# Kernel optimization log

Hardware: AMD Instinct MI355X
Metric: run time of the kernel (lower is better)

Reference implementation:

```python
import jax, jax.numpy as jnp
import numpy as np

N_EMBD = 1024  # C in forward; scale uses C**-0.5

def setup_inputs() -> dict:
    key = jax.random.key(0)
    k1, k2, k3, k4 = jax.random.split(key, 4)
    B, T, C, H = 4, 4096, N_EMBD, 64
    x = jax.random.normal(k1, (B, T, C), dtype=jnp.float32)
    # nn.Linear weights stored already-transposed as [in, out] for x @ W
    s = 1.0 / np.sqrt(C)
    Wq = jax.random.normal(k2, (C, H), dtype=jnp.float32) * s
    Wk = jax.random.normal(k3, (C, H), dtype=jnp.float32) * s
    Wv = jax.random.normal(k4, (C, H), dtype=jnp.float32) * s
    return {"x": x, "Wq": Wq, "Wk": Wk, "Wv": Wv}

def reference(x, Wq, Wk, Wv):
    B, T, C = x.shape
    q = jnp.einsum('btc,ch->bth', x, Wq)
    k = jnp.einsum('btc,ch->bth', x, Wk)
    v = jnp.einsum('btc,ch->bth', x, Wv)
    # scores scaled by C**-0.5 (note: original scales by embed dim, not head_size)
    wei = jnp.einsum('bth,bsh->bts', q, k) * (C ** -0.5)
    causal = jnp.tril(jnp.ones((T, T), dtype=bool))  # [T,T]
    wei = jnp.where(causal[None, :, :], wei, -jnp.inf)
    wei = jax.nn.softmax(wei, axis=-1)
    # dropout p=0.0 (eval-mode reference): identity
    out = jnp.einsum('bts,bsh->bth', wei, v)
    return out
```

## Files before the change

### kernel.cpp

```cpp
#include <hip/hip_runtime.h>

typedef __bf16 bf16x8 __attribute__((ext_vector_type(8)));
typedef float floatx16 __attribute__((ext_vector_type(16)));
typedef float floatx4 __attribute__((ext_vector_type(4)));

#define T_ 4096
#define STK 72
#define XSTR 40
#define NSPB 272

#define WT_OFF 0u
#define Q_OFF  393216u
#define K_OFF  2490368u
#define V_OFF  4587520u
#define OP_OFF 6684672u
#define ML_OFF 42336256u

__device__ __forceinline__ unsigned short bf16bits(float f) {
  __bf16 h = (__bf16)f;
  return __builtin_bit_cast(unsigned short, h);
}

__device__ __forceinline__ void async16(const void* g, void* l) {
  __builtin_amdgcn_global_load_lds((const __attribute__((address_space(1))) void*)g,
                                   (__attribute__((address_space(3))) void*)l, 16, 0, 0);
}

__global__ void wprep(const float* __restrict__ Wq, const float* __restrict__ Wk,
                      const float* __restrict__ Wv, __bf16* __restrict__ Wtg) {
  int idx = blockIdx.x * 256 + threadIdx.x;
  int mat = idx >> 16;
  int r = idx & 65535;
  int h = r & 63;
  int k = r >> 6;
  const float* W = (mat == 0) ? Wq : ((mat == 1) ? Wk : Wv);
  float v = W[k * 64 + h];
  if (mat == 0) v *= 0.03125f * 1.4426950408889634f;
  Wtg[(size_t)(mat * 64 + h) * 1024 + k] = (__bf16)v;
}

__global__ __launch_bounds__(256, 4) void proj(const float* __restrict__ x,
                                               const __bf16* __restrict__ Wtg,
                                               __bf16* __restrict__ Qp,
                                               __bf16* __restrict__ Kp,
                                               __bf16* __restrict__ Vp) {
  __shared__ __align__(16) unsigned short sm[2 * 16 * XSTR + 2 * 6144];
  unsigned short* xt = sm;
  unsigned short* wt = sm + 2 * 16 * XSTR;

  const int tid = threadIdx.x;
  const int wave = tid >> 6, lane = tid & 63;
  const int l15 = lane & 15, quad = lane >> 4;
  const size_t row0 = (size_t)blockIdx.x * 16;

  const int xrow = tid >> 3, xc4 = (tid & 7) * 4;
  const float* xsrc = (tid < 128) ? (x + (row0 + xrow) * 1024 + xc4) : x;
  const int wR0 = tid >> 2, wsl = tid & 3;

  floatx4 acc[3];
#pragma unroll
  for (int t = 0; t < 3; t++)
#pragma unroll
    for (int i = 0; i < 4; i++) acc[t][i] = 0.0f;

  {
    unsigned short* wb = wt;
#pragma unroll
    for (int i = 0; i < 3; i++) {
      int R = wR0 + i * 64;
      int sg = wsl ^ (R & 3);
      async16((const char*)Wtg + (size_t)R * 2048 + sg * 16,
              (char*)(wb + (i * 256 + wave * 64) * 8));
    }
    if (tid < 128) {
      float4 f = *(const float4*)(xsrc);
      unsigned short hb[4];
      hb[0] = bf16bits(f.x); hb[1] = bf16bits(f.y); hb[2] = bf16bits(f.z); hb[3] = bf16bits(f.w);
      *(uint2*)&xt[xrow * XSTR + xc4] = *(uint2*)(hb);
    }
  }
  __syncthreads();

  for (int kc = 0; kc < 32; ++kc) {
    const int cur = kc & 1;
    if (kc < 31) {
      unsigned short* wb = wt + (cur ^ 1) * 6144;
#pragma unroll
      for (int i = 0; i < 3; i++) {
        int R = wR0 + i * 64;
        int sg = wsl ^ (R & 3);
        async16((const char*)Wtg + (size_t)R * 2048 + (kc + 1) * 64 + sg * 16,
                (char*)(wb + (i * 256 + wave * 64) * 8));
      }
      if (tid < 128) {
        float4 f = *(const float4*)(xsrc + (kc + 1) * 32);
        unsigned short hb[4];
        hb[0] = bf16bits(f.x); hb[1] = bf16bits(f.y); hb[2] = bf16bits(f.z); hb[3] = bf16bits(f.w);
        *(uint2*)&xt[(cur ^ 1) * 16 * XSTR + xrow * XSTR + xc4] = *(uint2*)(hb);
      }
    }
    const unsigned short* xb = xt + cur * 16 * XSTR;
    const unsigned short* wb = wt + cur * 6144;
    bf16x8 a = *(const bf16x8*)&xb[l15 * XSTR + quad * 8];
#pragma unroll
    for (int ht = 0; ht < 3; ++ht) {
      int Rg = wave * 48 + ht * 16 + l15;
      bf16x8 b = *(const bf16x8*)&wb[Rg * 32 + ((quad ^ (Rg & 3))) * 8];
      acc[ht] = __builtin_amdgcn_mfma_f32_16x16x32_bf16(a, b, acc[ht], 0, 0, 0);
    }
    __syncthreads();
  }
#pragma unroll
  for (int ht = 0; ht < 3; ++ht) {
    int g0 = wave * 48 + ht * 16;
    int mat = g0 >> 6, h0 = g0 & 63;
    __bf16* outp = (mat == 0) ? Qp : ((mat == 1) ? Kp : Vp);
#pragma unroll
    for (int r = 0; r < 4; r++) {
      size_t row = row0 + quad * 4 + r;
      outp[row * 64 + h0 + l15] = (__bf16)acc[ht][r];
    }
  }
}

__global__ __launch_bounds__(256, 4) void attn1(const __bf16* __restrict__ Qp,
                                                const __bf16* __restrict__ Kp,
                                                const __bf16* __restrict__ Vp,
                                                float* __restrict__ Opart,
                                                float* __restrict__ mlpart) {
  __shared__ __align__(16) unsigned char smraw[36864];
  unsigned short* Vtl = (unsigned short*)smraw;
  unsigned short* Pl = Vtl + 64 * STK;
  float* Oe = (float*)smraw;

  const int tid = threadIdx.x;
  const int wave = tid >> 6, lane = tid & 63;
  const int l31 = lane & 31, half = lane >> 5;

  const int bid = blockIdx.x;
  const int b = bid / NSPB;
  const int f = bid - b * NSPB;
  int qt = 0, cum = 0;
  for (;;) { int s = (qt + 2) >> 1; if (f < cum + s) break; cum += s; qt++; }
  const int si = f - cum;
  const int S = (qt + 2) >> 1;
  const int n_iters = 2 * (qt + 1);
  const int bbase = n_iters / S, rem = n_iters % S;
  const int it0 = si * bbase + (si < rem ? si : rem);
  const int it1 = it0 + bbase + (si < rem ? 1 : 0);

  const int qb = qt * 128;
  const size_t brow = (size_t)b * 4096;

  bf16x8 qf[4];
  {
    const __bf16* qptr = Qp + (brow + qb + wave * 32 + l31) * 64 + half * 8;
#pragma unroll
    for (int ks = 0; ks < 4; ks++) qf[ks] = *(const bf16x8*)(qptr + ks * 16);
  }

  floatx16 o0, o1;
#pragma unroll
  for (int r = 0; r < 16; r++) { o0[r] = 0.0f; o1[r] = 0.0f; }
  float m_run = -1e30f, l_run = 0.0f;
  unsigned short* Pw = Pl + wave * 32 * STK;
  const int qrow = qb + wave * 32 + l31;

  const int vkp = tid & 31, vh0 = ((tid >> 5) & 7) * 8;
  const __bf16* vbase = Vp + brow * 64;

  {
    const __bf16* vp = vbase + (size_t)(it0 * 64 + 2 * vkp) * 64 + vh0;
    uint4 va4 = *(const uint4*)vp;
    uint4 vb4 = *(const uint4*)(vp + 64);
    const unsigned short* pa = (const unsigned short*)&va4;
    const unsigned short* pb = (const unsigned short*)&vb4;
#pragma unroll
    for (int j = 0; j < 8; j++) {
      unsigned int w = (unsigned int)pa[j] | ((unsigned int)pb[j] << 16);
      *(unsigned int*)&Vtl[(vh0 + j) * STK + 2 * vkp] = w;
    }
  }
  __syncthreads();

  for (int it = it0; it < it1; ++it) {
    const int k0 = it * 64;
    const bool hasnext = (it + 1 < it1);
    uint4 nva, nvb;
    if (hasnext) {
      const __bf16* vp = vbase + (size_t)((it + 1) * 64 + 2 * vkp) * 64 + vh0;
      nva = *(const uint4*)vp;
      nvb = *(const uint4*)(vp + 64);
    }
    const __bf16* kp0 = Kp + (brow + k0) * 64;
    floatx16 s0, s1;
#pragma unroll
    for (int r = 0; r < 16; r++) { s0[r] = 0.0f; s1[r] = 0.0f; }
#pragma unroll
    for (int ks = 0; ks < 4; ks++) {
      bf16x8 ka = *(const bf16x8*)(kp0 + l31 * 64 + ks * 16 + half * 8);
      bf16x8 kb = *(const bf16x8*)(kp0 + (32 + l31) * 64 + ks * 16 + half * 8);
      s0 = __builtin_amdgcn_mfma_f32_32x32x16_bf16(ka, qf[ks], s0, 0, 0, 0);
      s1 = __builtin_amdgcn_mfma_f32_32x32x16_bf16(kb, qf[ks], s1, 0, 0, 0);
    }
    if (k0 + 64 > qb) {
#pragma unroll
      for (int r = 0; r < 16; r++) {
        int rs = (r & 3) + 8 * (r >> 2) + 4 * half;
        if (k0 + rs > qrow) s0[r] = -1e30f;
        if (k0 + 32 + rs > qrow) s1[r] = -1e30f;
      }
    }
    float pm = -1e30f;
#pragma unroll
    for (int r = 0; r < 16; r++) { pm = fmaxf(pm, s0[r]); pm = fmaxf(pm, s1[r]); }
    pm = fmaxf(pm, __shfl_xor(pm, 32));
    float m_new = fmaxf(m_run, pm);
    float alpha = __builtin_amdgcn_exp2f(m_run - m_new);
    float psum = 0.0f;
#pragma unroll
    for (int r = 0; r < 16; r++) {
      s0[r] = __builtin_amdgcn_exp2f(s0[r] - m_new);
      s1[r] = __builtin_amdgcn_exp2f(s1[r] - m_new);
      psum += s0[r] + s1[r];
    }
    psum += __shfl_xor(psum, 32);
    l_run = l_run * alpha + psum;
    m_run = m_new;
#pragma unroll
    for (int r = 0; r < 16; r++) { o0[r] *= alpha; o1[r] *= alpha; }
#pragma unroll
    for (int g = 0; g < 4; ++g) {
      int kb0 = 8 * g + 4 * half;
      unsigned int w0 = (unsigned int)bf16bits(s0[4 * g]) | ((unsigned int)bf16bits(s0[4 * g + 1]) << 16);
      unsigned int w1 = (unsigned int)bf16bits(s0[4 * g + 2]) | ((unsigned int)bf16bits(s0[4 * g + 3]) << 16);
      *(uint2*)&Pw[l31 * STK + kb0] = make_uint2(w0, w1);
      unsigned int w2 = (unsigned int)bf16bits(s1[4 * g]) | ((unsigned int)bf16bits(s1[4 * g + 1]) << 16);
      unsigned int w3 = (unsigned int)bf16bits(s1[4 * g + 2]) | ((unsigned int)bf16bits(s1[4 * g + 3]) << 16);
      *(uint2*)&Pw[l31 * STK + 32 + kb0] = make_uint2(w2, w3);
    }
#pragma unroll
    for (int kst = 0; kst < 4; ++kst) {
      bf16x8 pf = *(const bf16x8*)&Pw[l31 * STK + kst * 16 + half * 8];
      bf16x8 va = *(const bf16x8*)&Vtl[l31 * STK + kst * 16 + half * 8];
      bf16x8 vb = *(const bf16x8*)&Vtl[(32 + l31) * STK + kst * 16 + half * 8];
      o0 = __builtin_amdgcn_mfma_f32_32x32x16_bf16(va, pf, o0, 0, 0, 0);
      o1 = __builtin_amdgcn_mfma_f32_32x32x16_bf16(vb, pf, o1, 0, 0, 0);
    }
    __syncthreads();
    if (hasnext) {
      const unsigned short* pa = (const unsigned short*)&nva;
      const unsigned short* pb = (const unsigned short*)&nvb;
#pragma unroll
      for (int j = 0; j < 8; j++) {
        unsigned int w = (unsigned int)pa[j] | ((unsigned int)pb[j] << 16);
        *(unsigned int*)&Vtl[(vh0 + j) * STK + 2 * vkp] = w;
      }
    }
    __syncthreads();
  }
#pragma unroll
  for (int r = 0; r < 16; r++) {
    int rs = (r & 3) + 8 * (r >> 2) + 4 * half;
    Oe[(wave * 32 + l31) * 68 + rs] = o0[r];
    Oe[(wave * 32 + l31) * 68 + 32 + rs] = o1[r];
  }
  if (lane < 32) {
    mlpart[(size_t)bid * 256 + wave * 32 + l31] = m_run;
    mlpart[(size_t)bid * 256 + 128 + wave * 32 + l31] = l_run;
  }
  __syncthreads();
  {
    float* dst = Opart + (size_t)bid * 8192;
    int r = tid >> 1, hh = (tid & 1) * 32;
#pragma unroll
    for (int i = 0; i < 8; i++)
      *(float4*)&dst[r * 64 + hh + 4 * i] = *(float4*)&Oe[r * 68 + hh + 4 * i];
  }
}

__global__ __launch_bounds__(256, 4) void attn2(const float* __restrict__ Opart,
                                                const float* __restrict__ mlpart,
                                                float* __restrict__ out) {
  const int bid = blockIdx.x;
  const int b = bid >> 7, rg = bid & 127;
  const int qt = rg >> 2;
  int cum = 0;
  for (int i = 0; i < qt; i++) cum += (i + 2) >> 1;
  const int S = (qt + 2) >> 1;
  const int t = threadIdx.x;
  const int r = t >> 3;
  const int prow = (rg & 3) * 32 + r;
  const int h0 = (t & 7) * 8;

  float M = -1e30f;
  for (int s = 0; s < S; s++)
    M = fmaxf(M, mlpart[(size_t)(b * NSPB + cum + s) * 256 + prow]);
  float a[8];
#pragma unroll
  for (int i = 0; i < 8; i++) a[i] = 0.0f;
  float L = 0.0f;
  for (int s = 0; s < S; s++) {
    size_t pb = (size_t)(b * NSPB + cum + s);
    float w = __builtin_amdgcn_exp2f(mlpart[pb * 256 + prow] - M);
    L += w * mlpart[pb * 256 + 128 + prow];
    const float* op = Opart + pb * 8192 + prow * 64 + h0;
    float4 v0 = *(const float4*)op;
    float4 v1 = *(const float4*)(op + 4);
    a[0] += w * v0.x; a[1] += w * v0.y; a[2] += w * v0.z; a[3] += w * v0.w;
    a[4] += w * v1.x; a[5] += w * v1.y; a[6] += w * v1.z; a[7] += w * v1.w;
  }
  float inv = 1.0f / L;
  float* po = out + ((size_t)b * 4096 + rg * 32 + r) * 64 + h0;
  float4 r0, r1;
  r0.x = a[0] * inv; r0.y = a[1] * inv; r0.z = a[2] * inv; r0.w = a[3] * inv;
  r1.x = a[4] * inv; r1.y = a[5] * inv; r1.z = a[6] * inv; r1.w = a[7] * inv;
  *(float4*)po = r0;
  *(float4*)(po + 4) = r1;
}

extern "C" void kernel_launch(void* const* d_in, const int* in_sizes, int n_in,
                              void* d_out, int out_size, void* d_ws, size_t ws_size,
                              hipStream_t stream) {
  (void)in_sizes; (void)n_in; (void)out_size; (void)ws_size;
  const float* x = (const float*)d_in[0];
  const float* Wq = (const float*)d_in[1];
  const float* Wk = (const float*)d_in[2];
  const float* Wv = (const float*)d_in[3];
  char* ws = (char*)d_ws;
  __bf16* Wtg = (__bf16*)(ws + WT_OFF);
  __bf16* Qp = (__bf16*)(ws + Q_OFF);
  __bf16* Kp = (__bf16*)(ws + K_OFF);
  __bf16* Vp = (__bf16*)(ws + V_OFF);
  float* Opart = (float*)(ws + OP_OFF);
  float* mlp = (float*)(ws + ML_OFF);
  float* out = (float*)d_out;

  hipLaunchKernelGGL(wprep, dim3(768), dim3(256), 0, stream, Wq, Wk, Wv, Wtg);
  hipLaunchKernelGGL(proj, dim3(1024), dim3(256), 0, stream, x, Wtg, Qp, Kp, Vp);
  hipLaunchKernelGGL(attn1, dim3(4 * NSPB), dim3(256), 0, stream, Qp, Kp, Vp, Opart, mlp);
  hipLaunchKernelGGL(attn2, dim3(512), dim3(256), 0, stream, Opart, mlp, out);
}
```

Measured before the change: 182.3 us.

## Pre-transpose V globally and keep P in registers via lane shuffles

Adds a separate kernel that writes V transposed to workspace, so the attention kernel loads V fragments directly from global memory instead of staging and transposing them through LDS each iteration. The softmax probabilities are now packed to bf16 in registers and exchanged between the two wave halves with shuffles, replacing the LDS write/read round trip. This removes both per-iteration block barriers. In exchange it costs an extra kernel launch, extra global traffic for the transposed V, and more registers, so the occupancy hint drops from 4 to 3 blocks.

```diff
diff --git a/kernel.cpp b/kernel.cpp
--- a/kernel.cpp
+++ b/kernel.cpp
@@ -5,7 +5,6 @@
 typedef float floatx4 __attribute__((ext_vector_type(4)));
 
 #define T_ 4096
-#define STK 72
 #define XSTR 40
 #define NSPB 272
 
@@ -15,6 +14,7 @@
 #define V_OFF  4587520u
 #define OP_OFF 6684672u
 #define ML_OFF 42336256u
+#define VT_OFF 44040192u
 
 __device__ __forceinline__ unsigned short bf16bits(float f) {
   __bf16 h = (__bf16)f;
@@ -123,15 +123,30 @@
   }
 }
 
-__global__ __launch_bounds__(256, 4) void attn1(const __bf16* __restrict__ Qp,
+__global__ __launch_bounds__(256) void vtr(const __bf16* __restrict__ Vp,
+                                           __bf16* __restrict__ Vt) {
+  __shared__ __align__(16) unsigned short tl[64 * 72];
+  const int tid = threadIdx.x;
+  const int bb = blockIdx.x >> 6, tt = blockIdx.x & 63;
+  const __bf16* src = Vp + ((size_t)bb * 4096 + tt * 64) * 64;
+  int row = tid >> 2, c16 = (tid & 3) * 16;
+  *(uint4*)&tl[row * 72 + c16] = *(const uint4*)(src + row * 64 + c16);
+  *(uint4*)&tl[row * 72 + c16 + 8] = *(const uint4*)(src + row * 64 + c16 + 8);
+  __syncthreads();
+  unsigned short ob[16];
+#pragma unroll
+  for (int i = 0; i < 16; i++) ob[i] = tl[(c16 + i) * 72 + row];
+  __bf16* dst = Vt + (size_t)bb * 262144 + (size_t)row * 4096 + tt * 64 + c16;
+  *(uint4*)dst = *(uint4*)(ob);
+  *(uint4*)(dst + 8) = *(uint4*)(ob + 8);
+}
+
+__global__ __launch_bounds__(256, 3) void attn1(const __bf16* __restrict__ Qp,
                                                 const __bf16* __restrict__ Kp,
-                                                const __bf16* __restrict__ Vp,
+                                                const __bf16* __restrict__ Vt,
                                                 float* __restrict__ Opart,
                                                 float* __restrict__ mlpart) {
-  __shared__ __align__(16) unsigned char smraw[36864];
-  unsigned short* Vtl = (unsigned short*)smraw;
-  unsigned short* Pl = Vtl + 64 * STK;
-  float* Oe = (float*)smraw;
+  __shared__ __align__(16) float Oe[128 * 68];
 
   const int tid = threadIdx.x;
   const int wave = tid >> 6, lane = tid & 63;
@@ -163,45 +178,30 @@
 #pragma unroll
   for (int r = 0; r < 16; r++) { o0[r] = 0.0f; o1[r] = 0.0f; }
   float m_run = -1e30f, l_run = 0.0f;
-  unsigned short* Pw = Pl + wave * 32 * STK;
   const int qrow = qb + wave * 32 + l31;
 
-  const int vkp = tid & 31, vh0 = ((tid >> 5) & 7) * 8;
-  const __bf16* vbase = Vp + brow * 64;
-
-  {
-    const __bf16* vp = vbase + (size_t)(it0 * 64 + 2 * vkp) * 64 + vh0;
-    uint4 va4 = *(const uint4*)vp;
-    uint4 vb4 = *(const uint4*)(vp + 64);
-    const unsigned short* pa = (const unsigned short*)&va4;
-    const unsigned short* pb = (const unsigned short*)&vb4;
-#pragma unroll
-    for (int j = 0; j < 8; j++) {
-      unsigned int w = (unsigned int)pa[j] | ((unsigned int)pb[j] << 16);
-      *(unsigned int*)&Vtl[(vh0 + j) * STK + 2 * vkp] = w;
-    }
-  }
-  __syncthreads();
+  const __bf16* kbase = Kp + brow * 64;
+  const __bf16* vb0 = Vt + (size_t)b * 262144 + (size_t)l31 * 4096 + half * 8;
+  const __bf16* vb1 = vb0 + 32 * 4096;
 
   for (int it = it0; it < it1; ++it) {
     const int k0 = it * 64;
-    const bool hasnext = (it + 1 < it1);
-    uint4 nva, nvb;
-    if (hasnext) {
-      const __bf16* vp = vbase + (size_t)((it + 1) * 64 + 2 * vkp) * 64 + vh0;
-      nva = *(const uint4*)vp;
-      nvb = *(const uint4*)(vp + 64);
-    }
-    const __bf16* kp0 = Kp + (brow + k0) * 64;
+    const __bf16* kp0 = kbase + (size_t)k0 * 64 + half * 8;
     floatx16 s0, s1;
 #pragma unroll
     for (int r = 0; r < 16; r++) { s0[r] = 0.0f; s1[r] = 0.0f; }
 #pragma unroll
     for (int ks = 0; ks < 4; ks++) {
-      bf16x8 ka = *(const bf16x8*)(kp0 + l31 * 64 + ks * 16 + half * 8);
-      bf16x8 kb = *(const bf16x8*)(kp0 + (32 + l31) * 64 + ks * 16 + half * 8);
+      bf16x8 ka = *(const bf16x8*)(kp0 + l31 * 64 + ks * 16);
+      bf16x8 kb = *(const bf16x8*)(kp0 + (32 + l31) * 64 + ks * 16);
       s0 = __builtin_amdgcn_mfma_f32_32x32x16_bf16(ka, qf[ks], s0, 0, 0, 0);
       s1 = __builtin_amdgcn_mfma_f32_32x32x16_bf16(kb, qf[ks], s1, 0, 0, 0);
+    }
+    bf16x8 vfa[4], vfb[4];
+#pragma unroll
+    for (int kst = 0; kst < 4; kst++) {
+      vfa[kst] = *(const bf16x8*)(vb0 + k0 + kst * 16);
+      vfb[kst] = *(const bf16x8*)(vb1 + k0 + kst * 16);
     }
     if (k0 + 64 > qb) {
 #pragma unroll
@@ -229,35 +229,27 @@
     m_run = m_new;
 #pragma unroll
     for (int r = 0; r < 16; r++) { o0[r] *= alpha; o1[r] *= alpha; }
-#pragma unroll
-    for (int g = 0; g < 4; ++g) {
-      int kb0 = 8 * g + 4 * half;
-      unsigned int w0 = (unsigned int)bf16bits(s0[4 * g]) | ((unsigned int)bf16bits(s0[4 * g + 1]) << 16);
-      unsigned int w1 = (unsigned int)bf16bits(s0[4 * g + 2]) | ((unsigned int)bf16bits(s0[4 * g + 3]) << 16);
-      *(uint2*)&Pw[l31 * STK + kb0] = make_uint2(w0, w1);
-      unsigned int w2 = (unsigned int)bf16bits(s1[4 * g]) | ((unsigned int)bf16bits(s1[4 * g + 1]) << 16);
-      unsigned int w3 = (unsigned int)bf16bits(s1[4 * g + 2]) | ((unsigned int)bf16bits(s1[4 * g + 3]) << 16);
-      *(uint2*)&Pw[l31 * STK + 32 + kb0] = make_uint2(w2, w3);
+    unsigned int pk0[8], pk1[8];
+#pragma unroll
+    for (int m = 0; m < 8; m++) {
+      pk0[m] = (unsigned int)bf16bits(s0[2 * m]) | ((unsigned int)bf16bits(s0[2 * m + 1]) << 16);
+      pk1[m] = (unsigned int)bf16bits(s1[2 * m]) | ((unsigned int)bf16bits(s1[2 * m + 1]) << 16);
     }
 #pragma unroll
     for (int kst = 0; kst < 4; ++kst) {
-      bf16x8 pf = *(const bf16x8*)&Pw[l31 * STK + kst * 16 + half * 8];
-      bf16x8 va = *(const bf16x8*)&Vtl[l31 * STK + kst * 16 + half * 8];
-      bf16x8 vb = *(const bf16x8*)&Vtl[(32 + l31) * STK + kst * 16 + half * 8];
-      o0 = __builtin_amdgcn_mfma_f32_32x32x16_bf16(va, pf, o0, 0, 0, 0);
-      o1 = __builtin_amdgcn_mfma_f32_32x32x16_bf16(vb, pf, o1, 0, 0, 0);
-    }
-    __syncthreads();
-    if (hasnext) {
-      const unsigned short* pa = (const unsigned short*)&nva;
-      const unsigned short* pb = (const unsigned short*)&nvb;
-#pragma unroll
-      for (int j = 0; j < 8; j++) {
-        unsigned int w = (unsigned int)pa[j] | ((unsigned int)pb[j] << 16);
-        *(unsigned int*)&Vtl[(vh0 + j) * STK + 2 * vkp] = w;
-      }
-    }
-    __syncthreads();
+      const unsigned int* pkX = (kst < 2) ? pk0 : pk1;
+      int bb2 = 4 * (kst & 1);
+      unsigned int own0 = pkX[bb2 + 2 * half];
+      unsigned int own1 = pkX[bb2 + 2 * half + 1];
+      unsigned int u0 = pkX[bb2 + 2 * (1 - half)];
+      unsigned int u1 = pkX[bb2 + 2 * (1 - half) + 1];
+      unsigned int p0 = (unsigned int)__shfl_xor((int)u0, 32);
+      unsigned int p1 = (unsigned int)__shfl_xor((int)u1, 32);
+      uint4 fu = half ? make_uint4(p0, p1, own0, own1) : make_uint4(own0, own1, p0, p1);
+      bf16x8 pf = __builtin_bit_cast(bf16x8, fu);
+      o0 = __builtin_amdgcn_mfma_f32_32x32x16_bf16(vfa[kst], pf, o0, 0, 0, 0);
+      o1 = __builtin_amdgcn_mfma_f32_32x32x16_bf16(vfb[kst], pf, o1, 0, 0, 0);
+    }
   }
 #pragma unroll
   for (int r = 0; r < 16; r++) {
@@ -332,12 +324,14 @@
   __bf16* Qp = (__bf16*)(ws + Q_OFF);
   __bf16* Kp = (__bf16*)(ws + K_OFF);
   __bf16* Vp = (__bf16*)(ws + V_OFF);
+  __bf16* Vtp = (__bf16*)(ws + VT_OFF);
   float* Opart = (float*)(ws + OP_OFF);
   float* mlp = (float*)(ws + ML_OFF);
   float* out = (float*)d_out;
 
   hipLaunchKernelGGL(wprep, dim3(768), dim3(256), 0, stream, Wq, Wk, Wv, Wtg);
   hipLaunchKernelGGL(proj, dim3(1024), dim3(256), 0, stream, x, Wtg, Qp, Kp, Vp);
-  hipLaunchKernelGGL(attn1, dim3(4 * NSPB), dim3(256), 0, stream, Qp, Kp, Vp, Opart, mlp);
+  hipLaunchKernelGGL(vtr, dim3(256), dim3(256), 0, stream, Vp, Vtp);
+  hipLaunchKernelGGL(attn1, dim3(4 * NSPB), dim3(256), 0, stream, Qp, Kp, Vtp, Opart, mlp);
   hipLaunchKernelGGL(attn2, dim3(512), dim3(256), 0, stream, Opart, mlp, out);
 }
```

After: 190.8 us. +4.6%, slower.
